# Kernel tuning notes

Measured on AMD Instinct MI355X. Metric: run time of the kernel, lower is better.

## Reference

```python
import jax, jax.numpy as jnp
import numpy as np

NUM_HEADS = 16
NUM_KV_HEADS = 4
HEAD_DIM = 128
DIM = 2048
B, S = 2, 2048


def apply_rotary(t, cos, sin):
    # t: [B, S, H, D]; cos/sin: [S, D//2] -> broadcast [1, S, 1, D//2]
    tr = t.reshape(*t.shape[:-1], HEAD_DIM // 2, 2)
    t_r, t_i = tr[..., 0], tr[..., 1]
    c = cos[None, :, None, :]
    s = sin[None, :, None, :]
    o_r = t_r * c - t_i * s
    o_i = t_r * s + t_i * c
    return jnp.stack([o_r, o_i], axis=-1).reshape(t.shape)


def setup_inputs() -> dict:
    key = jax.random.key(0)
    ks = jax.random.split(key, 7)
    sc = 1.0 / np.sqrt(DIM)
    x = jax.random.normal(ks[0], (B, S, DIM), jnp.float32)
    pos = jnp.arange(S, dtype=jnp.float32)[:, None]
    inv_freq = 1.0 / (10000.0 ** (jnp.arange(0, HEAD_DIM, 2, dtype=jnp.float32) / HEAD_DIM))
    ang = pos * inv_freq[None, :]
    freqs_cos = jnp.cos(ang)
    freqs_sin = jnp.sin(ang)
    w_q = jax.random.normal(ks[1], (DIM, NUM_HEADS * HEAD_DIM), jnp.float32) * sc
    w_k = jax.random.normal(ks[2], (DIM, NUM_KV_HEADS * HEAD_DIM), jnp.float32) * sc
    w_v = jax.random.normal(ks[3], (DIM, NUM_KV_HEADS * HEAD_DIM), jnp.float32) * sc
    w_o = jax.random.normal(ks[4], (NUM_HEADS * HEAD_DIM, DIM), jnp.float32) * sc
    return {"x": x, "freqs_cos": freqs_cos, "freqs_sin": freqs_sin,
            "w_q": w_q, "w_k": w_k, "w_v": w_v, "w_o": w_o}


def reference(x, freqs_cos, freqs_sin, w_q, w_k, w_v, w_o):
    b, s, _ = x.shape
    kv_rep = NUM_HEADS // NUM_KV_HEADS
    q = (x @ w_q).reshape(b, s, NUM_HEADS, HEAD_DIM)
    k = (x @ w_k).reshape(b, s, NUM_KV_HEADS, HEAD_DIM)
    v = (x @ w_v).reshape(b, s, NUM_KV_HEADS, HEAD_DIM)
    q = apply_rotary(q, freqs_cos, freqs_sin)
    k = apply_rotary(k, freqs_cos, freqs_sin)
    # GQA: repeat KV heads to match query heads
    k = jnp.repeat(k, kv_rep, axis=2)
    v = jnp.repeat(v, kv_rep, axis=2)
    scores = jnp.einsum('bqhd,bkhd->bhqk', q, k) / np.sqrt(HEAD_DIM)
    causal = jnp.triu(jnp.full((s, s), -jnp.inf, jnp.float32), k=1)
    scores = scores + causal[None, None, :, :]
    attn = jax.nn.softmax(scores, axis=-1)
    out = jnp.einsum('bhqk,bkhd->bqhd', attn, v).reshape(b, s, NUM_HEADS * HEAD_DIM)
    return out @ w_o
```

## Files before the change

### kernel.cpp

```cpp
#include <hip/hip_runtime.h>
#include <stdint.h>

#define DIMSZ 2048
#define NH 16
#define NKV 4
#define HD 128
#define BATCH 2
#define SEQ 2048
#define MROWS (BATCH*SEQ)
#define NQKV (NH*HD + 2*NKV*HD)

typedef unsigned short u16;
typedef float f32x4 __attribute__((ext_vector_type(4)));
typedef short short8 __attribute__((ext_vector_type(8)));
typedef __bf16 bf16x8 __attribute__((ext_vector_type(8)));
typedef unsigned short u16x4 __attribute__((ext_vector_type(4)));
typedef unsigned short u16x8 __attribute__((ext_vector_type(8)));

__device__ __forceinline__ u16 f2bf(float f) {
  __bf16 h = (__bf16)f;
  return __builtin_bit_cast(u16, h);
}

__device__ __forceinline__ float bf2f(u16 h) {
  union { uint32_t u; float f; } v; v.u = ((uint32_t)h) << 16; return v.f;
}

__device__ __forceinline__ void async16(void* lds, const void* g) {
  __builtin_amdgcn_global_load_lds(
      (const __attribute__((address_space(1))) void*)(g),
      (__attribute__((address_space(3))) void*)(lds), 16, 0, 0);
}

__device__ __forceinline__ bf16x8 load_frag(const u16* p) {
  short8 v = *reinterpret_cast<const short8*>(p);
  return __builtin_bit_cast(bf16x8, v);
}

__global__ __launch_bounds__(256) void prep_kernel(const float* __restrict__ x,
                                                   const float* __restrict__ wq,
                                                   const float* __restrict__ wk,
                                                   const float* __restrict__ wv,
                                                   const float* __restrict__ wo,
                                                   u16* __restrict__ xb,
                                                   u16* __restrict__ wtqkv,
                                                   u16* __restrict__ wto) {
  __shared__ float tb[64][65];
  int y = blockIdx.y;
  if (y >= 80) {
    int id = (y - 80) * 32 + blockIdx.x;
    int i = (id * 256 + (int)threadIdx.x) * 4;
    float4 v = *reinterpret_cast<const float4*>(x + i);
    u16x4 o;
    o.x = f2bf(v.x); o.y = f2bf(v.y); o.z = f2bf(v.z); o.w = f2bf(v.w);
    *reinterpret_cast<u16x4*>(xb + i) = o;
    return;
  }
  const float* src; int srcN; u16* dst; int nbase;
  if (y < 32)      { src = wq; srcN = 2048; dst = wtqkv;                        nbase = y * 64; }
  else if (y < 40) { src = wk; srcN = 512;  dst = wtqkv + (size_t)2048 * 2048;  nbase = (y - 32) * 64; }
  else if (y < 48) { src = wv; srcN = 512;  dst = wtqkv + (size_t)2560 * 2048;  nbase = (y - 40) * 64; }
  else             { src = wo; srcN = 2048; dst = wto;                          nbase = (y - 48) * 64; }
  int k0 = blockIdx.x * 64;
  int t = threadIdx.x;
  int lr = t >> 4, lc = (t & 15) * 4;
#pragma unroll
  for (int i = 0; i < 4; ++i) {
    int row = lr + i * 16;
    float4 v = *reinterpret_cast<const float4*>(&src[(size_t)(k0 + row) * srcN + nbase + lc]);
    tb[row][lc] = v.x; tb[row][lc + 1] = v.y; tb[row][lc + 2] = v.z; tb[row][lc + 3] = v.w;
  }
  __syncthreads();
  int n = t >> 3, kg = (t & 7) * 8;
#pragma unroll
  for (int i = 0; i < 2; ++i) {
    int nn = n + i * 32;
    u16x8 o;
#pragma unroll
    for (int j = 0; j < 8; ++j) o[j] = f2bf(tb[kg + j][nn]);
    *reinterpret_cast<u16x8*>(&dst[(size_t)(nbase + nn) * 2048 + k0 + kg]) = o;
  }
}

#define COMPUTE_PAIR(q)                                                              \
  {                                                                                  \
    bf16x8 af[2][2];                                                                 \
    _Pragma("unroll")                                                                \
    for (int m2 = 0; m2 < 2; ++m2)                                                   \
      _Pragma("unroll")                                                              \
      for (int kk = 0; kk < 2; ++kk)                                                 \
        af[m2][kk] = load_frag(&lds[buf][0][wm * 8192 +                              \
            (((q) * 2 + m2) * 16 + l16) * 64 + ((kk * 4 + lg) ^ (l16 & 7)) * 8]);    \
    __builtin_amdgcn_s_setprio(1);                                                   \
    _Pragma("unroll")                                                                \
    for (int m2 = 0; m2 < 2; ++m2)                                                   \
      _Pragma("unroll")                                                              \
      for (int ni = 0; ni < 4; ++ni)                                                 \
        _Pragma("unroll")                                                            \
        for (int kk = 0; kk < 2; ++kk)                                               \
          acc[(q) * 2 + m2][ni] = __builtin_amdgcn_mfma_f32_16x16x32_bf16(           \
              af[m2][kk], bper[ni][kk], acc[(q) * 2 + m2][ni], 0, 0, 0);             \
    __builtin_amdgcn_s_setprio(0);                                                   \
  }

template <bool BF16OUT>
__global__ __launch_bounds__(512, 2) void gemm8p_kernel(const u16* __restrict__ A,
                                                        const u16* __restrict__ BT,
                                                        void* __restrict__ Cp,
                                                        int M, int N, int K, int gx) {
  __shared__ u16 lds[2][2][16384];
  const int tid = threadIdx.x;
  const int wave = tid >> 6, lane = tid & 63;
  const int l16 = lane & 15, lg = lane >> 4;
  const int wm = wave >> 2, wn = wave & 3;
  const int rloc = lane >> 3;
  const int sOff = ((lane & 7) ^ rloc) * 8;
  const int nwg = gridDim.x;
  const int swz = (blockIdx.x & 7) * (nwg >> 3) + (blockIdx.x >> 3);
  const int bm = (swz / gx) * 256, bn = (swz % gx) * 256;

  f32x4 acc[8][4] = {};

  auto stage = [&](int dstbuf, int x, int h, const u16* xp, int xr0, int kk0) {
#pragma unroll
    for (int j = 0; j < 2; ++j) {
      int c = j * 8 + wave;
      async16(&lds[dstbuf][x][h * 8192 + c * 512],
              xp + (size_t)(xr0 + h * 128 + c * 8 + rloc) * K + kk0 + sOff);
    }
  };

  stage(0, 0, 0, A, bm, 0);
  stage(0, 0, 1, A, bm, 0);
  stage(0, 1, 0, BT, bn, 0);
  stage(0, 1, 1, BT, bn, 0);

  const int NT = K >> 6;
  for (int kt = 0; kt < NT; ++kt) {
    const int buf = kt & 1, nbuf = buf ^ 1;
    const int k0n = (kt + 1) << 6;
    const bool pf = (kt + 1 < NT);
    bf16x8 bper[4][2];

    if (pf) {
      stage(nbuf, 0, 0, A, bm, k0n);
      asm volatile("s_waitcnt vmcnt(2)" ::: "memory");
    } else {
      asm volatile("s_waitcnt vmcnt(0)" ::: "memory");
    }
    __builtin_amdgcn_s_barrier();
    __builtin_amdgcn_sched_barrier(0);
#pragma unroll
    for (int ni = 0; ni < 4; ++ni)
#pragma unroll
      for (int kk = 0; kk < 2; ++kk)
        bper[ni][kk] = load_frag(&lds[buf][1][(wn >> 1) * 8192 +
            ((wn & 1) * 64 + ni * 16 + l16) * 64 + ((kk * 4 + lg) ^ (l16 & 7)) * 8]);
    COMPUTE_PAIR(0)
    if (pf) stage(nbuf, 0, 1, A, bm, k0n);
    __builtin_amdgcn_s_barrier();
    __builtin_amdgcn_sched_barrier(0);
    COMPUTE_PAIR(1)
    if (pf) stage(nbuf, 1, 0, BT, bn, k0n);
    __builtin_amdgcn_s_barrier();
    __builtin_amdgcn_sched_barrier(0);
    COMPUTE_PAIR(2)
    if (pf) stage(nbuf, 1, 1, BT, bn, k0n);
    __builtin_amdgcn_s_barrier();
    __builtin_amdgcn_sched_barrier(0);
    COMPUTE_PAIR(3)
    __builtin_amdgcn_s_barrier();
  }

#pragma unroll
  for (int mi = 0; mi < 8; ++mi)
#pragma unroll
    for (int ni = 0; ni < 4; ++ni)
#pragma unroll
      for (int r = 0; r < 4; ++r) {
        size_t idx = (size_t)(bm + wm * 128 + mi * 16 + lg * 4 + r) * N +
                     bn + wn * 64 + ni * 16 + l16;
        if (BF16OUT) ((u16*)Cp)[idx] = f2bf(acc[mi][ni][r]);
        else         ((float*)Cp)[idx] = acc[mi][ni][r];
      }
}

#define COMPUTE_MB(q)                                                                \
  {                                                                                  \
    bf16x8 af[2];                                                                    \
    _Pragma("unroll")                                                                \
    for (int kk = 0; kk < 2; ++kk)                                                   \
      af[kk] = load_frag(&lds2[buf][(wm * 64 + (q) * 16 + l16) * 64 +                \
                                    ((kk * 4 + lg) ^ (l16 & 7)) * 8]);               \
    __builtin_amdgcn_s_setprio(1);                                                   \
    _Pragma("unroll")                                                                \
    for (int ni = 0; ni < 4; ++ni)                                                   \
      _Pragma("unroll")                                                              \
      for (int kk = 0; kk < 2; ++kk)                                                 \
        acc[(q)][ni] = __builtin_amdgcn_mfma_f32_16x16x32_bf16(                      \
            af[kk], bper[ni][kk], acc[(q)][ni], 0, 0, 0);                            \
    __builtin_amdgcn_s_setprio(0);                                                   \
  }

__global__ __launch_bounds__(512, 2) void gemm8p_n128_kernel(const u16* __restrict__ A,
                                                             const u16* __restrict__ BT,
                                                             float* __restrict__ C,
                                                             int M, int N, int K, int gx) {
  __shared__ u16 lds2[2][24576];
  const int tid = threadIdx.x;
  const int wave = tid >> 6, lane = tid & 63;
  const int l16 = lane & 15, lg = lane >> 4;
  const int wm = wave >> 1, wn = wave & 1;
  const int rloc = lane >> 3;
  const int sOff = ((lane & 7) ^ rloc) * 8;
  const int nwg = gridDim.x;
  const int swz = (blockIdx.x & 7) * (nwg >> 3) + (blockIdx.x >> 3);
  const int bm = (swz / gx) * 256, bn = (swz % gx) * 128;

  f32x4 acc[4][4] = {};

  auto stageA = [&](int dstbuf, int h, int kk0) {
#pragma unroll
    for (int j = 0; j < 2; ++j) {
      int c = j * 8 + wave;
      async16(&lds2[dstbuf][h * 8192 + c * 512],
              A + (size_t)(bm + h * 128 + c * 8 + rloc) * K + kk0 + sOff);
    }
  };
  auto stageB = [&](int dstbuf, int kk0) {
#pragma unroll
    for (int j = 0; j < 2; ++j) {
      int c = j * 8 + wave;
      async16(&lds2[dstbuf][16384 + c * 512],
              BT + (size_t)(bn + c * 8 + rloc) * K + kk0 + sOff);
    }
  };

  stageA(0, 0, 0);
  stageA(0, 1, 0);
  stageB(0, 0);

  const int NT = K >> 6;
  for (int kt = 0; kt < NT; ++kt) {
    const int buf = kt & 1, nbuf = buf ^ 1;
    const int k0n = (kt + 1) << 6;
    const bool pf = (kt + 1 < NT);
    bf16x8 bper[4][2];

    if (pf) {
      stageA(nbuf, 0, k0n);
      asm volatile("s_waitcnt vmcnt(2)" ::: "memory");
    } else {
      asm volatile("s_waitcnt vmcnt(0)" ::: "memory");
    }
    __builtin_amdgcn_s_barrier();
    __builtin_amdgcn_sched_barrier(0);
#pragma unroll
    for (int ni = 0; ni < 4; ++ni)
#pragma unroll
      for (int kk = 0; kk < 2; ++kk)
        bper[ni][kk] = load_frag(&lds2[buf][16384 +
            (wn * 64 + ni * 16 + l16) * 64 + ((kk * 4 + lg) ^ (l16 & 7)) * 8]);
    COMPUTE_MB(0)
    if (pf) stageA(nbuf, 1, k0n);
    __builtin_amdgcn_s_barrier();
    __builtin_amdgcn_sched_barrier(0);
    COMPUTE_MB(1)
    if (pf) stageB(nbuf, k0n);
    __builtin_amdgcn_s_barrier();
    __builtin_amdgcn_sched_barrier(0);
    COMPUTE_MB(2)
    __builtin_amdgcn_s_barrier();
    __builtin_amdgcn_sched_barrier(0);
    COMPUTE_MB(3)
    __builtin_amdgcn_s_barrier();
  }

#pragma unroll
  for (int mb = 0; mb < 4; ++mb)
#pragma unroll
    for (int ni = 0; ni < 4; ++ni)
#pragma unroll
      for (int r = 0; r < 4; ++r)
        C[(size_t)(bm + wm * 64 + mb * 16 + lg * 4 + r) * N +
          bn + wn * 64 + ni * 16 + l16] = acc[mb][ni][r];
}

__global__ __launch_bounds__(256) void rv_kernel(const u16* __restrict__ qkv,
                                                 const float* __restrict__ fc,
                                                 const float* __restrict__ fs,
                                                 u16* __restrict__ Kb,
                                                 u16* __restrict__ vt) {
  __shared__ u16 t[32][33];
  int bid = blockIdx.x;
  if (bid < 4096) {
    int kh = bid >> 10;
    int gi = (bid & 1023) * 256 + (int)threadIdx.x;
    int i = gi & 63;
    int tt = gi >> 6;
    int s = tt & (SEQ - 1), b = tt >> 11;
    float c = fc[s * 64 + i], sn = fs[s * 64 + i];
    uint32_t pr = *reinterpret_cast<const uint32_t*>(&qkv[(size_t)tt * NQKV + NH * HD + kh * HD + 2 * i]);
    float tr = bf2f((u16)(pr & 0xffff)), ti = bf2f((u16)(pr >> 16));
    uint32_t w = (uint32_t)f2bf(tr * c - ti * sn) |
                 ((uint32_t)f2bf(tr * sn + ti * c) << 16);
    *reinterpret_cast<uint32_t*>(&Kb[((size_t)(b * NKV + kh) * SEQ + s) * HD + 2 * i]) = w;
    return;
  }
  int id = bid - 4096;
  int bk = id >> 8;
  int rem = id & 255;
  int s0 = (rem >> 2) * 32;
  int d0 = (rem & 3) * 32;
  int b = bk >> 2, kh = bk & 3;
  int tx = threadIdx.x & 31, ty = threadIdx.x >> 5;
#pragma unroll
  for (int i = 0; i < 4; ++i) {
    int row = ty + i * 8;
    t[row][tx] = qkv[(size_t)(b * SEQ + s0 + row) * NQKV + NH * HD + NKV * HD + kh * HD + d0 + tx];
  }
  __syncthreads();
#pragma unroll
  for (int i = 0; i < 4; ++i) {
    int row = ty + i * 8;
    vt[((size_t)(b * NKV + kh) * HD + d0 + row) * SEQ + s0 + tx] = t[tx][row];
  }
}

__global__ __launch_bounds__(256) void attn_kernel(const u16* __restrict__ qkv,
                                                   const float* __restrict__ fc,
                                                   const float* __restrict__ fs,
                                                   const u16* __restrict__ Kc,
                                                   const u16* __restrict__ VT,
                                                   u16* __restrict__ AO) {
  __shared__ u16 Ks[2][64 * 128];
  __shared__ u16 Vs[2][128 * 64];
  __shared__ u16 Ps[4][16 * 64];
  const int pairi = blockIdx.x;
  const int h = blockIdx.y, b = blockIdx.z;
  const int kvh = h >> 2;
  const int tid = threadIdx.x, wave = tid >> 6, lane = tid & 63;
  const int l16 = lane & 15, lg = lane >> 4;

  const u16* Kbase = Kc + (size_t)(b * NKV + kvh) * SEQ * HD;
  const u16* Vbase = VT + (size_t)(b * NKV + kvh) * HD * SEQ;

  bf16x8 onesf;
#pragma unroll
  for (int j = 0; j < 8; ++j) onesf[j] = __builtin_bit_cast(__bf16, (u16)0x3F80);

  int kOff[4], vOff[4], kDst[4], vDst[4];
#pragma unroll
  for (int i = 0; i < 4; ++i) {
    int chunk = i * 4 + wave;
    int krow = chunk * 4 + (lane >> 4);
    kOff[i] = krow * HD + ((lane & 15) ^ (krow & 15)) * 8;
    kDst[i] = chunk * 512;
    int vrow = chunk * 8 + (lane >> 3);
    vOff[i] = vrow * SEQ + ((lane & 7) ^ (vrow & 7)) * 8;
    vDst[i] = chunk * 512;
  }

  for (int sel = 0; sel < 2; ++sel) {
    const int qblk = sel ? pairi : (31 - pairi);
    const int qrow0 = qblk * 64 + wave * 16;
    const int rq = qrow0 + l16;

    const float qs = 0.12751689760098266f;
    const u16* Qrow = qkv + (size_t)(b * SEQ + rq) * NQKV + h * HD;
    const float* fcb = fc + (size_t)rq * 64;
    const float* fsb = fs + (size_t)rq * 64;
    bf16x8 qf[4];
#pragma unroll
    for (int c = 0; c < 4; ++c) {
      bf16x8 raw = load_frag(Qrow + c * 32 + lg * 8);
      float4 cc = *reinterpret_cast<const float4*>(fcb + c * 16 + lg * 4);
      float4 sv = *reinterpret_cast<const float4*>(fsb + c * 16 + lg * 4);
      bf16x8 q;
#pragma unroll
      for (int j = 0; j < 4; ++j) {
        float e = (float)raw[2 * j], od = (float)raw[2 * j + 1];
        float ce = (&cc.x)[j] * qs, se = (&sv.x)[j] * qs;
        q[2 * j]     = (__bf16)(e * ce - od * se);
        q[2 * j + 1] = (__bf16)(e * se + od * ce);
      }
      qf[c] = q;
    }

    f32x4 o[8] = {};
    f32x4 lsum = {};
    float m = -3e38f;

    __syncthreads();
#pragma unroll
    for (int i = 0; i < 4; ++i) {
      async16(&Ks[0][kDst[i]], Kbase + kOff[i]);
      async16(&Vs[0][vDst[i]], Vbase + vOff[i]);
    }

    for (int kt = 0; kt <= qblk; ++kt) {
      const int cur = kt & 1;
      __syncthreads();
      if (kt < qblk) {
        const int k0n = (kt + 1) * 64;
#pragma unroll
        for (int i = 0; i < 4; ++i) {
          async16(&Ks[cur ^ 1][kDst[i]], Kbase + (size_t)k0n * HD + kOff[i]);
          async16(&Vs[cur ^ 1][vDst[i]], Vbase + k0n + vOff[i]);
        }
      }

      f32x4 s[4] = {};
      __builtin_amdgcn_s_setprio(1);
#pragma unroll
      for (int cb = 0; cb < 4; ++cb) {
#pragma unroll
        for (int c = 0; c < 4; ++c) {
          bf16x8 kf = load_frag(&Ks[cur][(cb * 16 + l16) * 128 + (((c * 4 + lg) ^ l16) & 15) * 8]);
          s[cb] = __builtin_amdgcn_mfma_f32_16x16x32_bf16(kf, qf[c], s[cb], 0, 0, 0);
        }
      }
      __builtin_amdgcn_s_setprio(0);

      if (kt == qblk) {
        const int k0 = kt * 64;
#pragma unroll
        for (int cb = 0; cb < 4; ++cb) {
#pragma unroll
          for (int r = 0; r < 4; ++r) {
            int key = k0 + cb * 16 + lg * 4 + r;
            if (key > rq) s[cb][r] = -1e30f;
          }
        }
      }

      float v0 = fmaxf(fmaxf(fmaxf(s[0][0], s[0][1]), fmaxf(s[0][2], s[0][3])),
                       fmaxf(fmaxf(s[1][0], s[1][1]), fmaxf(s[1][2], s[1][3])));
      v0 = fmaxf(v0, fmaxf(fmaxf(fmaxf(s[2][0], s[2][1]), fmaxf(s[2][2], s[2][3])),
                           fmaxf(fmaxf(s[3][0], s[3][1]), fmaxf(s[3][2], s[3][3]))));
      v0 = fmaxf(v0, __shfl_xor(v0, 16));
      v0 = fmaxf(v0, __shfl_xor(v0, 32));

      bool need = v0 > m + 8.f;
      if (__any(need)) {
        float newm = fmaxf(m, v0);
        float sc = exp2f(m - newm);
        m = newm;
        float scR[4];
#pragma unroll
        for (int r = 0; r < 4; ++r) scR[r] = __shfl(sc, lg * 4 + r);
#pragma unroll
        for (int r = 0; r < 4; ++r) {
          lsum[r] *= scR[r];
#pragma unroll
          for (int db = 0; db < 8; ++db) o[db][r] *= scR[r];
        }
      }

#pragma unroll
      for (int cb = 0; cb < 4; ++cb) {
        uint32_t lo = (uint32_t)f2bf(exp2f(s[cb][0] - m)) |
                      ((uint32_t)f2bf(exp2f(s[cb][1] - m)) << 16);
        uint32_t hi = (uint32_t)f2bf(exp2f(s[cb][2] - m)) |
                      ((uint32_t)f2bf(exp2f(s[cb][3] - m)) << 16);
        int idx = (l16 * 64 + cb * 16 + lg * 4) ^ ((l16 & 7) << 3);
        uint64_t w = (uint64_t)lo | ((uint64_t)hi << 32);
        *reinterpret_cast<uint64_t*>(&Ps[wave][idx]) = w;
      }

      bf16x8 pf[2];
#pragma unroll
      for (int c = 0; c < 2; ++c)
        pf[c] = load_frag(&Ps[wave][(l16 * 64 + c * 32 + lg * 8) ^ ((l16 & 7) << 3)]);
      __builtin_amdgcn_s_setprio(1);
#pragma unroll
      for (int c = 0; c < 2; ++c)
        lsum = __builtin_amdgcn_mfma_f32_16x16x32_bf16(pf[c], onesf, lsum, 0, 0, 0);
#pragma unroll
      for (int db = 0; db < 8; ++db) {
#pragma unroll
        for (int c = 0; c < 2; ++c) {
          bf16x8 vf = load_frag(&Vs[cur][(db * 16 + l16) * 64 + ((c * 4 + lg) ^ (l16 & 7)) * 8]);
          o[db] = __builtin_amdgcn_mfma_f32_16x16x32_bf16(pf[c], vf, o[db], 0, 0, 0);
        }
      }
      __builtin_amdgcn_s_setprio(0);
    }

#pragma unroll
    for (int r = 0; r < 4; ++r) {
      float inv = 1.f / lsum[r];
      int rqo = qrow0 + lg * 4 + r;
      size_t dst = ((size_t)(b * SEQ + rqo) * NH + h) * HD;
#pragma unroll
      for (int db = 0; db < 8; ++db)
        AO[dst + db * 16 + l16] = f2bf(o[db][r] * inv);
    }
  }
}

extern "C" void kernel_launch(void* const* d_in, const int* in_sizes, int n_in,
                              void* d_out, int out_size, void* d_ws, size_t ws_size,
                              hipStream_t stream) {
  (void)in_sizes; (void)n_in; (void)out_size; (void)ws_size;
  const float* x  = (const float*)d_in[0];
  const float* fc = (const float*)d_in[1];
  const float* fs = (const float*)d_in[2];
  const float* wq = (const float*)d_in[3];
  const float* wk = (const float*)d_in[4];
  const float* wv = (const float*)d_in[5];
  const float* wo = (const float*)d_in[6];
  float* out = (float*)d_out;

  char* ws = (char*)d_ws;
  u16*  xb    = (u16*)(ws);
  u16*  wtqkv = (u16*)(ws + 16777216);
  u16*  wto   = (u16*)(ws + 29360128);
  u16*  qkv   = (u16*)(ws + 37748736);
  u16*  Kb    = (u16*)(ws + 62914560);
  u16*  VTb   = (u16*)(ws + 67108864);
  u16*  AOb   = (u16*)(ws + 71303168);

  prep_kernel<<<dim3(32, 336), dim3(256), 0, stream>>>(x, wq, wk, wv, wo, xb, wtqkv, wto);

  gemm8p_kernel<true><<<dim3(192), dim3(512), 0, stream>>>(xb, wtqkv, qkv, MROWS, NQKV, DIMSZ, 12);

  rv_kernel<<<dim3(6144), dim3(256), 0, stream>>>(qkv, fc, fs, Kb, VTb);

  attn_kernel<<<dim3(16, 16, 2), dim3(256), 0, stream>>>(qkv, fc, fs, Kb, VTb, AOb);

  gemm8p_n128_kernel<<<dim3(256), dim3(512), 0, stream>>>(AOb, wto, out, MROWS, DIMSZ, DIMSZ, 16);
}
```

Baseline: 193.4 us.

## Restructure attention into one q-block per workgroup with single-buffered V tile

Each workgroup now handles a single 64-row query block, launched heaviest-first over a flat 1024-block grid, replacing the earlier scheme where each workgroup processed a paired heavy/light block. V is now single-buffered and loaded at the start of each key tile, overlapping the QK^T MFMAs, with explicit vmcnt waits and barriers. P is written and consumed in two 32-key halves to shrink the per-wave P buffer. Together these cut LDS use, which is meant to raise occupancy and balance load. The cost is an extra barrier per tile and V-load latency that is no longer hidden by a full tile of prefetch.

New measurement: 195.1 us. About the same (+0.8%).

```diff
diff --git a/kernel.cpp b/kernel.cpp
--- a/kernel.cpp
+++ b/kernel.cpp
@@ -334,13 +334,17 @@
                                                    const u16* __restrict__ VT,
                                                    u16* __restrict__ AO) {
   __shared__ u16 Ks[2][64 * 128];
-  __shared__ u16 Vs[2][128 * 64];
-  __shared__ u16 Ps[4][16 * 64];
-  const int pairi = blockIdx.x;
-  const int h = blockIdx.y, b = blockIdx.z;
+  __shared__ u16 Vs[128 * 64];
+  __shared__ u16 Ps[4][16 * 32];
+  const int bid = blockIdx.x;
+  const int qblk = 31 - (bid >> 5);
+  const int bh = bid & 31;
+  const int b = bh >> 4, h = bh & 15;
   const int kvh = h >> 2;
   const int tid = threadIdx.x, wave = tid >> 6, lane = tid & 63;
   const int l16 = lane & 15, lg = lane >> 4;
+  const int qrow0 = qblk * 64 + wave * 16;
+  const int rq = qrow0 + l16;
 
   const u16* Kbase = Kc + (size_t)(b * NKV + kvh) * SEQ * HD;
   const u16* Vbase = VT + (size_t)(b * NKV + kvh) * HD * SEQ;
@@ -361,141 +365,156 @@
     vDst[i] = chunk * 512;
   }
 
-  for (int sel = 0; sel < 2; ++sel) {
-    const int qblk = sel ? pairi : (31 - pairi);
-    const int qrow0 = qblk * 64 + wave * 16;
-    const int rq = qrow0 + l16;
-
-    const float qs = 0.12751689760098266f;
-    const u16* Qrow = qkv + (size_t)(b * SEQ + rq) * NQKV + h * HD;
-    const float* fcb = fc + (size_t)rq * 64;
-    const float* fsb = fs + (size_t)rq * 64;
-    bf16x8 qf[4];
-#pragma unroll
-    for (int c = 0; c < 4; ++c) {
-      bf16x8 raw = load_frag(Qrow + c * 32 + lg * 8);
-      float4 cc = *reinterpret_cast<const float4*>(fcb + c * 16 + lg * 4);
-      float4 sv = *reinterpret_cast<const float4*>(fsb + c * 16 + lg * 4);
-      bf16x8 q;
-#pragma unroll
-      for (int j = 0; j < 4; ++j) {
-        float e = (float)raw[2 * j], od = (float)raw[2 * j + 1];
-        float ce = (&cc.x)[j] * qs, se = (&sv.x)[j] * qs;
-        q[2 * j]     = (__bf16)(e * ce - od * se);
-        q[2 * j + 1] = (__bf16)(e * se + od * ce);
-      }
-      qf[c] = q;
-    }
-
-    f32x4 o[8] = {};
-    f32x4 lsum = {};
-    float m = -3e38f;
-
-    __syncthreads();
-#pragma unroll
-    for (int i = 0; i < 4; ++i) {
-      async16(&Ks[0][kDst[i]], Kbase + kOff[i]);
-      async16(&Vs[0][vDst[i]], Vbase + vOff[i]);
-    }
-
-    for (int kt = 0; kt <= qblk; ++kt) {
-      const int cur = kt & 1;
-      __syncthreads();
+  const float qs = 0.12751689760098266f;
+  const u16* Qrow = qkv + (size_t)(b * SEQ + rq) * NQKV + h * HD;
+  const float* fcb = fc + (size_t)rq * 64;
+  const float* fsb = fs + (size_t)rq * 64;
+  bf16x8 qf[4];
+#pragma unroll
+  for (int c = 0; c < 4; ++c) {
+    bf16x8 raw = load_frag(Qrow + c * 32 + lg * 8);
+    float4 cc = *reinterpret_cast<const float4*>(fcb + c * 16 + lg * 4);
+    float4 sv = *reinterpret_cast<const float4*>(fsb + c * 16 + lg * 4);
+    bf16x8 q;
+#pragma unroll
+    for (int j = 0; j < 4; ++j) {
+      float e = (float)raw[2 * j], od = (float)raw[2 * j + 1];
+      float ce = (&cc.x)[j] * qs, se = (&sv.x)[j] * qs;
+      q[2 * j]     = (__bf16)(e * ce - od * se);
+      q[2 * j + 1] = (__bf16)(e * se + od * ce);
+    }
+    qf[c] = q;
+  }
+
+  f32x4 o[8] = {};
+  f32x4 lsum = {};
+  float m = -3e38f;
+
+#pragma unroll
+  for (int i = 0; i < 4; ++i) async16(&Ks[0][kDst[i]], Kbase + kOff[i]);
+
+  for (int kt = 0; kt <= qblk; ++kt) {
+    const int cur = kt & 1;
+    asm volatile("s_waitcnt vmcnt(0)" ::: "memory");
+    __builtin_amdgcn_s_barrier();
+    __builtin_amdgcn_sched_barrier(0);
+    {
+      const int k0 = kt * 64;
+#pragma unroll
+      for (int i = 0; i < 4; ++i) async16(&Vs[vDst[i]], Vbase + k0 + vOff[i]);
       if (kt < qblk) {
         const int k0n = (kt + 1) * 64;
 #pragma unroll
-        for (int i = 0; i < 4; ++i) {
+        for (int i = 0; i < 4; ++i)
           async16(&Ks[cur ^ 1][kDst[i]], Kbase + (size_t)k0n * HD + kOff[i]);
-          async16(&Vs[cur ^ 1][vDst[i]], Vbase + k0n + vOff[i]);
+      }
+    }
+
+    f32x4 s[4] = {};
+    __builtin_amdgcn_s_setprio(1);
+#pragma unroll
+    for (int cb = 0; cb < 4; ++cb) {
+#pragma unroll
+      for (int c = 0; c < 4; ++c) {
+        bf16x8 kf = load_frag(&Ks[cur][(cb * 16 + l16) * 128 + (((c * 4 + lg) ^ l16) & 15) * 8]);
+        s[cb] = __builtin_amdgcn_mfma_f32_16x16x32_bf16(kf, qf[c], s[cb], 0, 0, 0);
+      }
+    }
+    __builtin_amdgcn_s_setprio(0);
+
+    if (kt == qblk) {
+      const int k0 = kt * 64;
+#pragma unroll
+      for (int cb = 0; cb < 4; ++cb) {
+#pragma unroll
+        for (int r = 0; r < 4; ++r) {
+          int key = k0 + cb * 16 + lg * 4 + r;
+          if (key > rq) s[cb][r] = -1e30f;
         }
       }
-
-      f32x4 s[4] = {};
+    }
+
+    float v0 = fmaxf(fmaxf(fmaxf(s[0][0], s[0][1]), fmaxf(s[0][2], s[0][3])),
+                     fmaxf(fmaxf(s[1][0], s[1][1]), fmaxf(s[1][2], s[1][3])));
+    v0 = fmaxf(v0, fmaxf(fmaxf(fmaxf(s[2][0], s[2][1]), fmaxf(s[2][2], s[2][3])),
+                         fmaxf(fmaxf(s[3][0], s[3][1]), fmaxf(s[3][2], s[3][3]))));
+    v0 = fmaxf(v0, __shfl_xor(v0, 16));
+    v0 = fmaxf(v0, __shfl_xor(v0, 32));
+
+    bool need = v0 > m + 8.f;
+    if (__any(need)) {
+      float newm = fmaxf(m, v0);
+      float sc = exp2f(m - newm);
+      m = newm;
+      float scR[4];
+#pragma unroll
+      for (int r = 0; r < 4; ++r) scR[r] = __shfl(sc, lg * 4 + r);
+#pragma unroll
+      for (int r = 0; r < 4; ++r) {
+        lsum[r] *= scR[r];
+#pragma unroll
+        for (int db = 0; db < 8; ++db) o[db][r] *= scR[r];
+      }
+    }
+
+#pragma unroll
+    for (int cb = 0; cb < 2; ++cb) {
+      uint32_t lo = (uint32_t)f2bf(exp2f(s[cb][0] - m)) |
+                    ((uint32_t)f2bf(exp2f(s[cb][1] - m)) << 16);
+      uint32_t hi = (uint32_t)f2bf(exp2f(s[cb][2] - m)) |
+                    ((uint32_t)f2bf(exp2f(s[cb][3] - m)) << 16);
+      uint64_t w = (uint64_t)lo | ((uint64_t)hi << 32);
+      *reinterpret_cast<uint64_t*>(&Ps[wave][l16 * 32 + cb * 16 + lg * 4]) = w;
+    }
+
+    if (kt < qblk) { asm volatile("s_waitcnt vmcnt(4)" ::: "memory"); }
+    else           { asm volatile("s_waitcnt vmcnt(0)" ::: "memory"); }
+    __builtin_amdgcn_s_barrier();
+    __builtin_amdgcn_sched_barrier(0);
+
+    {
+      bf16x8 pf = load_frag(&Ps[wave][l16 * 32 + lg * 8]);
       __builtin_amdgcn_s_setprio(1);
-#pragma unroll
-      for (int cb = 0; cb < 4; ++cb) {
-#pragma unroll
-        for (int c = 0; c < 4; ++c) {
-          bf16x8 kf = load_frag(&Ks[cur][(cb * 16 + l16) * 128 + (((c * 4 + lg) ^ l16) & 15) * 8]);
-          s[cb] = __builtin_amdgcn_mfma_f32_16x16x32_bf16(kf, qf[c], s[cb], 0, 0, 0);
-        }
+      lsum = __builtin_amdgcn_mfma_f32_16x16x32_bf16(pf, onesf, lsum, 0, 0, 0);
+#pragma unroll
+      for (int db = 0; db < 8; ++db) {
+        bf16x8 vf = load_frag(&Vs[(db * 16 + l16) * 64 + ((lg) ^ (l16 & 7)) * 8]);
+        o[db] = __builtin_amdgcn_mfma_f32_16x16x32_bf16(pf, vf, o[db], 0, 0, 0);
       }
       __builtin_amdgcn_s_setprio(0);
-
-      if (kt == qblk) {
-        const int k0 = kt * 64;
-#pragma unroll
-        for (int cb = 0; cb < 4; ++cb) {
-#pragma unroll
-          for (int r = 0; r < 4; ++r) {
-            int key = k0 + cb * 16 + lg * 4 + r;
-            if (key > rq) s[cb][r] = -1e30f;
-          }
-        }
-      }
-
-      float v0 = fmaxf(fmaxf(fmaxf(s[0][0], s[0][1]), fmaxf(s[0][2], s[0][3])),
-                       fmaxf(fmaxf(s[1][0], s[1][1]), fmaxf(s[1][2], s[1][3])));
-      v0 = fmaxf(v0, fmaxf(fmaxf(fmaxf(s[2][0], s[2][1]), fmaxf(s[2][2], s[2][3])),
-                           fmaxf(fmaxf(s[3][0], s[3][1]), fmaxf(s[3][2], s[3][3]))));
-      v0 = fmaxf(v0, __shfl_xor(v0, 16));
-      v0 = fmaxf(v0, __shfl_xor(v0, 32));
-
-      bool need = v0 > m + 8.f;
-      if (__any(need)) {
-        float newm = fmaxf(m, v0);
-        float sc = exp2f(m - newm);
-        m = newm;
-        float scR[4];
-#pragma unroll
-        for (int r = 0; r < 4; ++r) scR[r] = __shfl(sc, lg * 4 + r);
-#pragma unroll
-        for (int r = 0; r < 4; ++r) {
-          lsum[r] *= scR[r];
-#pragma unroll
-          for (int db = 0; db < 8; ++db) o[db][r] *= scR[r];
-        }
-      }
-
-#pragma unroll
-      for (int cb = 0; cb < 4; ++cb) {
-        uint32_t lo = (uint32_t)f2bf(exp2f(s[cb][0] - m)) |
-                      ((uint32_t)f2bf(exp2f(s[cb][1] - m)) << 16);
-        uint32_t hi = (uint32_t)f2bf(exp2f(s[cb][2] - m)) |
-                      ((uint32_t)f2bf(exp2f(s[cb][3] - m)) << 16);
-        int idx = (l16 * 64 + cb * 16 + lg * 4) ^ ((l16 & 7) << 3);
-        uint64_t w = (uint64_t)lo | ((uint64_t)hi << 32);
-        *reinterpret_cast<uint64_t*>(&Ps[wave][idx]) = w;
-      }
-
-      bf16x8 pf[2];
-#pragma unroll
-      for (int c = 0; c < 2; ++c)
-        pf[c] = load_frag(&Ps[wave][(l16 * 64 + c * 32 + lg * 8) ^ ((l16 & 7) << 3)]);
+    }
+
+#pragma unroll
+    for (int cb = 2; cb < 4; ++cb) {
+      uint32_t lo = (uint32_t)f2bf(exp2f(s[cb][0] - m)) |
+                    ((uint32_t)f2bf(exp2f(s[cb][1] - m)) << 16);
+      uint32_t hi = (uint32_t)f2bf(exp2f(s[cb][2] - m)) |
+                    ((uint32_t)f2bf(exp2f(s[cb][3] - m)) << 16);
+      uint64_t w = (uint64_t)lo | ((uint64_t)hi << 32);
+      *reinterpret_cast<uint64_t*>(&Ps[wave][l16 * 32 + (cb - 2) * 16 + lg * 4]) = w;
+    }
+
+    {
+      bf16x8 pf = load_frag(&Ps[wave][l16 * 32 + lg * 8]);
       __builtin_amdgcn_s_setprio(1);
-#pragma unroll
-      for (int c = 0; c < 2; ++c)
-        lsum = __builtin_amdgcn_mfma_f32_16x16x32_bf16(pf[c], onesf, lsum, 0, 0, 0);
+      lsum = __builtin_amdgcn_mfma_f32_16x16x32_bf16(pf, onesf, lsum, 0, 0, 0);
 #pragma unroll
       for (int db = 0; db < 8; ++db) {
-#pragma unroll
-        for (int c = 0; c < 2; ++c) {
-          bf16x8 vf = load_frag(&Vs[cur][(db * 16 + l16) * 64 + ((c * 4 + lg) ^ (l16 & 7)) * 8]);
-          o[db] = __builtin_amdgcn_mfma_f32_16x16x32_bf16(pf[c], vf, o[db], 0, 0, 0);
-        }
+        bf16x8 vf = load_frag(&Vs[(db * 16 + l16) * 64 + ((4 + lg) ^ (l16 & 7)) * 8]);
+        o[db] = __builtin_amdgcn_mfma_f32_16x16x32_bf16(pf, vf, o[db], 0, 0, 0);
       }
       __builtin_amdgcn_s_setprio(0);
     }
-
-#pragma unroll
-    for (int r = 0; r < 4; ++r) {
-      float inv = 1.f / lsum[r];
-      int rqo = qrow0 + lg * 4 + r;
-      size_t dst = ((size_t)(b * SEQ + rqo) * NH + h) * HD;
-#pragma unroll
-      for (int db = 0; db < 8; ++db)
-        AO[dst + db * 16 + l16] = f2bf(o[db][r] * inv);
-    }
+  }
+
+#pragma unroll
+  for (int r = 0; r < 4; ++r) {
+    float inv = 1.f / lsum[r];
+    int rqo = qrow0 + lg * 4 + r;
+    size_t dst = ((size_t)(b * SEQ + rqo) * NH + h) * HD;
+#pragma unroll
+    for (int db = 0; db < 8; ++db)
+      AO[dst + db * 16 + l16] = f2bf(o[db][r] * inv);
   }
 }
 
@@ -527,7 +546,7 @@
 
   rv_kernel<<<dim3(6144), dim3(256), 0, stream>>>(qkv, fc, fs, Kb, VTb);
 
-  attn_kernel<<<dim3(16, 16, 2), dim3(256), 0, stream>>>(qkv, fc, fs, Kb, VTb, AOb);
+  attn_kernel<<<dim3(1024), dim3(256), 0, stream>>>(qkv, fc, fs, Kb, VTb, AOb);
 
   gemm8p_n128_kernel<<<dim3(256), dim3(512), 0, stream>>>(AOb, wto, out, MROWS, DIMSZ, DIMSZ, 16);
 }
```
